# Performance work log

Hardware: AMD Instinct MI355X
Metric: run time of the kernel (lower is better)

The kernel has to match this reference:

```python
import jax, jax.numpy as jnp
import numpy as np

B, T, D, DI, K, M, H, HD, L, VOCAB = 8, 512, 256, 512, 4, 2, 4, 64, 2, 272


def rmsnorm(x, w, eps=1e-6):
    return x * jax.lax.rsqrt(jnp.mean(x * x, axis=-1, keepdims=True) + eps) * w


def rotate_half(x):
    x1, x2 = x[..., ::2], x[..., 1::2]
    return jnp.stack([-x2, x1], axis=-1).reshape(x.shape)


def causal_conv(x, w, b):
    # x: [B,T,C], w: [C,K] depthwise causal conv, then silu
    y = jax.lax.conv_general_dilated(
        x.transpose(0, 2, 1), w[:, None, :],
        window_strides=(1,), padding=[(K - 1, 0)],
        feature_group_count=x.shape[-1])
    return jax.nn.silu(y.transpose(0, 2, 1) + b)


def delta_memory(x, Wv, Wg, Wb, Wa, A_log, dt_bias, Wblend, Wout):
    # x: [B,T,D]; per-timestep delta-rule fast-weight update with decay + key rotation
    Bv, Tn, Dm = x.shape
    vals = (x @ Wv).reshape(Bv, Tn, M, H, HD)
    gate = jax.nn.sigmoid(x @ Wg)                                   # [B,T,H]
    beta = jax.nn.sigmoid(jnp.einsum('btd,mdh->btmh', x, Wb))       # [B,T,M,H]
    alpha = jnp.einsum('btd,mdh->btmh', x, Wa) + dt_bias            # [B,T,M,H]
    decay = jnp.exp(-jnp.exp(A_log)[None, None] * jax.nn.softplus(alpha))
    blend = jax.nn.softmax((x @ Wblend).reshape(Bv, Tn, H, M), axis=-1)
    rk0 = x.reshape(Bv, Tn, H, HD)
    rk0 = rk0 / jnp.maximum(jnp.linalg.norm(rk0, axis=-1, keepdims=True), 1e-12)
    rks = [rk0]
    for _ in range(M - 1):
        rks.append(rotate_half(rks[-1]))
    rks = jnp.stack(rks, axis=2)                                    # [B,T,M,H,d]
    wks = jnp.pad(rks[:, :-1], ((0, 0), (1, 0), (0, 0), (0, 0), (0, 0)))  # shifted keys

    def step(S, inp):
        v, wk, rk, bt, dc, bl, g = inp
        S = S * dc[..., None, None]                                  # [B,M,H,d,d]
        pred = jnp.einsum('bmhdk,bmhd->bmhk', S, wk)
        err = (v - pred) * bt[..., None]
        S = S + wk[..., None] * err[..., None, :]                    # outer-product write
        read = jnp.einsum('bmhdk,bmhd->bmhk', S, rk)
        o = jnp.einsum('bhm,bmhk->bhk', bl, read) * g[..., None]
        return S, o

    tf = lambda a: jnp.moveaxis(a, 1, 0)
    xs = (tf(vals), tf(wks), tf(rks), tf(beta), tf(decay), tf(blend), tf(gate))
    S0 = jnp.zeros((Bv, M, H, HD, HD), x.dtype)
    _, o = jax.lax.scan(step, S0, xs)                                # [T,B,H,d]
    o = jnp.moveaxis(o, 0, 1).reshape(Bv, Tn, Dm)
    return x + o @ Wout


def setup_inputs():
    key = jax.random.key(0)
    ks = jax.random.split(key, 16)
    n = lambda k, shape, sc=0.02: jax.random.normal(k, shape, jnp.float32) * sc
    return {
        'ids': jax.random.randint(ks[0], (B, T), 0, VOCAB, jnp.int32),
        'emb': n(ks[1], (VOCAB, D)),
        'norm_w': jnp.ones((L, D), jnp.float32),
        'W_up': n(ks[2], (L, D, DI)),
        'W_gate': n(ks[3], (L, D, DI)),
        'W_down': n(ks[4], (L, DI, D)),
        'conv_w': n(ks[5], (L, DI, K), 0.1),
        'conv_b': jnp.zeros((L, DI), jnp.float32),
        'Wv': n(ks[6], (L, D, M * D)),
        'Wg': n(ks[7], (L, D, H)),
        'Wb': n(ks[8], (L, M, D, H)),
        'Wa': n(ks[9], (L, M, D, H)),
        'A_log': n(ks[10], (L, M, H), 0.5),
        'dt_bias': n(ks[11], (L, M, H), 0.5),
        'Wblend': n(ks[12], (L, D, H * M)),
        'Wout': n(ks[13], (L, D, D)),
        'final_norm_w': jnp.ones((D,), jnp.float32),
    }


def reference(ids, emb, norm_w, W_up, W_gate, W_down, conv_w, conv_b,
              Wv, Wg, Wb, Wa, A_log, dt_bias, Wblend, Wout, final_norm_w):
    x = emb[ids]
    for l in range(L):
        nx = rmsnorm(x, norm_w[l])
        h = causal_conv(nx @ W_up[l], conv_w[l], conv_b[l])
        out = (jax.nn.silu(nx @ W_gate[l]) * h) @ W_down[l]
        out = delta_memory(out, Wv[l], Wg[l], Wb[l], Wa[l],
                           A_log[l], dt_bias[l], Wblend[l], Wout[l])
        x = x + out
    return rmsnorm(x, final_norm_w) @ emb.T  # tied head
```

## Files before the change

### kernel.cpp

```cpp
#include <hip/hip_runtime.h>
#include <math.h>

#define BB 8
#define TT 512
#define DD 256
#define DIM 512
#define KW 4
#define MM 2
#define HH 4
#define HDIM 64
#define LL 2
#define VV 272

typedef __attribute__((ext_vector_type(8))) short bf16x8;
typedef __attribute__((ext_vector_type(4))) float f32x4;

__device__ __forceinline__ float sigf(float x){ return 1.f/(1.f+__expf(-x)); }
__device__ __forceinline__ float siluf(float x){ return x/(1.f+__expf(-x)); }

__device__ __forceinline__ unsigned short f2bf(float f){
  unsigned int u = __float_as_uint(f);
  unsigned int r = (u + 0x7FFFu + ((u >> 16) & 1u)) >> 16;
  return (unsigned short)r;
}
__device__ __forceinline__ float bf2f(unsigned short s){
  return __uint_as_float(((unsigned int)s) << 16);
}

__device__ __forceinline__ float xor1_add(float x){
  int y = __builtin_amdgcn_update_dpp(0, __float_as_int(x), 0xB1, 0xF, 0xF, true);
  return x + __int_as_float(y);
}
__device__ __forceinline__ float xor2_add(float x){
  int y = __builtin_amdgcn_update_dpp(0, __float_as_int(x), 0x4E, 0xF, 0xF, true);
  return x + __int_as_float(y);
}
__device__ __forceinline__ float ror4_add(float x){
  int y = __builtin_amdgcn_update_dpp(0, __float_as_int(x), 0x124, 0xF, 0xF, true);
  return x + __int_as_float(y);
}
__device__ __forceinline__ float ror8_add(float x){
  int y = __builtin_amdgcn_update_dpp(0, __float_as_int(x), 0x128, 0xF, 0xF, true);
  return x + __int_as_float(y);
}

__device__ __forceinline__ void gl_lds16(const void* g, void* l){
  __builtin_amdgcn_global_load_lds(
      (const __attribute__((address_space(1))) unsigned int*)g,
      (__attribute__((address_space(3))) unsigned int*)l,
      16, 0, 0);
}

#define LWB 589824
__global__ void k_cvt(const float* __restrict__ Wup, const float* __restrict__ Wgate,
                      const float* __restrict__ Wdown, const float* __restrict__ Wv,
                      const float* __restrict__ Wout, const float* __restrict__ emb,
                      const float* __restrict__ normw, const float* __restrict__ fnw,
                      unsigned short* __restrict__ wbf){
  int idx = blockIdx.x*256 + threadIdx.x;
  if (idx >= 2*LWB + VV*DD) return;
  float v;
  if (idx < 2*LWB){
    int l = (idx >= LWB) ? 1 : 0;
    int local = idx - l*LWB;
    if (local < 131072){ int n = local>>8, k = local&255;
      v = Wup[(size_t)l*131072 + k*DIM + n];
      if (l == 1) v *= normw[DD + k]; }
    else if (local < 262144){ local -= 131072; int n = local>>8, k = local&255;
      v = Wgate[(size_t)l*131072 + k*DIM + n];
      if (l == 1) v *= normw[DD + k]; }
    else if (local < 393216){ local -= 262144; int n = local>>9, k = local&511;
      v = Wdown[(size_t)l*131072 + k*DD + n]; }
    else if (local < 524288){ local -= 393216; int n = local>>8, k = local&255;
      v = Wv[(size_t)l*131072 + k*DIM + n]; }
    else { local -= 524288; int n = local>>8, k = local&255;
      v = Wout[(size_t)l*65536 + k*DD + n]; }
  } else {
    int k = (idx - 2*LWB) & 255;
    v = emb[idx - 2*LWB] * fnw[k];
  }
  wbf[idx] = f2bf(v);
}

__global__ void __launch_bounds__(256) k_embed_norm(const int* __restrict__ ids,
                                                    const float* __restrict__ emb,
                                                    const float* __restrict__ w,
                                                    float* __restrict__ x,
                                                    unsigned short* __restrict__ out){
  const int wv = threadIdx.x >> 6, l = threadIdx.x & 63;
  const int row = blockIdx.x*4 + wv;
  float4 v = *(const float4*)&emb[(size_t)ids[row]*DD + l*4];
  *(float4*)&x[(size_t)row*DD + l*4] = v;
  float ss = v.x*v.x + v.y*v.y + v.z*v.z + v.w*v.w;
  #pragma unroll
  for (int o = 32; o > 0; o >>= 1) ss += __shfl_xor(ss, o, 64);
  float sc = rsqrtf(ss*(1.f/DD) + 1e-6f);
  float4 wvv = *(const float4*)&w[l*4];
  ushort4 r;
  r.x = f2bf(v.x*sc*wvv.x); r.y = f2bf(v.y*sc*wvv.y);
  r.z = f2bf(v.z*sc*wvv.z); r.w = f2bf(v.w*sc*wvv.w);
  *(ushort4*)&out[(size_t)row*DD + l*4] = r;
}

template<int MODE>
__global__ void __launch_bounds__(256) k_gemm64(const unsigned short* __restrict__ A,
                                                const unsigned short* __restrict__ Bt,
                                                float* __restrict__ Cf,
                                                unsigned short* __restrict__ Cb,
                                                int N, int K){
  __shared__ unsigned short as[64][72];
  __shared__ unsigned short bs[64][72];
  const int tid = threadIdx.x;
  const int w = tid >> 6, l = tid & 63;
  const int m0 = blockIdx.y*64, n0 = blockIdx.x*64;
  const int ar = tid >> 2, ac = (tid & 3)*16;
  f32x4 acc[4] = {};
  for (int k0 = 0; k0 < K; k0 += 64){
    { const bf16x8* src = (const bf16x8*)&A[(size_t)(m0+ar)*K + k0 + ac];
      *(bf16x8*)&as[ar][ac]   = src[0];
      *(bf16x8*)&as[ar][ac+8] = src[1];
    }
    { int n = n0 + ar;
      bf16x8 z; z = (bf16x8)(short)0;
      bf16x8 b0 = z, b1 = z;
      if (n < N){
        const bf16x8* src = (const bf16x8*)&Bt[(size_t)n*K + k0 + ac];
        b0 = src[0]; b1 = src[1];
      }
      *(bf16x8*)&bs[ar][ac]   = b0;
      *(bf16x8*)&bs[ar][ac+8] = b1;
    }
    __syncthreads();
    const int mr = w*16 + (l & 15);
    const int kb = (l >> 4)*8;
    #pragma unroll
    for (int kc2 = 0; kc2 < 2; ++kc2){
      bf16x8 af = *(const bf16x8*)&as[mr][kc2*32 + kb];
      #pragma unroll
      for (int nt = 0; nt < 4; ++nt){
        bf16x8 bfr = *(const bf16x8*)&bs[nt*16 + (l & 15)][kc2*32 + kb];
        acc[nt] = __builtin_amdgcn_mfma_f32_16x16x32_bf16(af, bfr, acc[nt], 0, 0, 0);
      }
    }
    __syncthreads();
  }
  #pragma unroll
  for (int nt = 0; nt < 4; ++nt){
    int col = n0 + nt*16 + (l & 15);
    if (col < N){
      #pragma unroll
      for (int r = 0; r < 4; ++r){
        int row = m0 + w*16 + (l >> 4)*4 + r;
        if (MODE == 0 || MODE == 2) Cf[(size_t)row*N + col] = acc[nt][r];
        if (MODE == 1 || MODE == 2) Cb[(size_t)row*N + col] = f2bf(acc[nt][r]);
      }
    }
  }
}

__global__ void __launch_bounds__(256) k_gemmlogit(const float* __restrict__ X,
                                                   const float* __restrict__ pssq,
                                                   const unsigned short* __restrict__ Bt,
                                                   float* __restrict__ Cf,
                                                   int N, int K){
  __shared__ unsigned short as[64][72];
  __shared__ unsigned short bs[64][72];
  const int tid = threadIdx.x;
  const int w = tid >> 6, l = tid & 63;
  const int m0 = blockIdx.y*64, n0 = blockIdx.x*64;
  const int ar = tid >> 2, ac = (tid & 3)*16;
  const int arow = m0 + ar;
  const int ROWS = BB*TT;
  float ssq = pssq[arow] + pssq[ROWS + arow] + pssq[2*ROWS + arow] + pssq[3*ROWS + arow];
  const float sc = rsqrtf(ssq*(1.f/DD) + 1e-6f);
  f32x4 acc[4] = {};
  for (int k0 = 0; k0 < K; k0 += 64){
    { const float* src = &X[(size_t)arow*K + k0 + ac];
      #pragma unroll
      for (int j = 0; j < 4; ++j){
        float4 a = *(const float4*)&src[j*4];
        ushort4 u = make_ushort4(f2bf(a.x*sc), f2bf(a.y*sc), f2bf(a.z*sc), f2bf(a.w*sc));
        *(ushort4*)&as[ar][ac + j*4] = u;
      }
    }
    { int n = n0 + ar;
      bf16x8 z; z = (bf16x8)(short)0;
      bf16x8 b0 = z, b1 = z;
      if (n < N){
        const bf16x8* src = (const bf16x8*)&Bt[(size_t)n*K + k0 + ac];
        b0 = src[0]; b1 = src[1];
      }
      *(bf16x8*)&bs[ar][ac]   = b0;
      *(bf16x8*)&bs[ar][ac+8] = b1;
    }
    __syncthreads();
    const int mr = w*16 + (l & 15);
    const int kb = (l >> 4)*8;
    #pragma unroll
    for (int kc2 = 0; kc2 < 2; ++kc2){
      bf16x8 af = *(const bf16x8*)&as[mr][kc2*32 + kb];
      #pragma unroll
      for (int nt = 0; nt < 4; ++nt){
        bf16x8 bfr = *(const bf16x8*)&bs[nt*16 + (l & 15)][kc2*32 + kb];
        acc[nt] = __builtin_amdgcn_mfma_f32_16x16x32_bf16(af, bfr, acc[nt], 0, 0, 0);
      }
    }
    __syncthreads();
  }
  #pragma unroll
  for (int nt = 0; nt < 4; ++nt){
    int col = n0 + nt*16 + (l & 15);
    if (col < N){
      #pragma unroll
      for (int r = 0; r < 4; ++r){
        int row = m0 + w*16 + (l >> 4)*4 + r;
        Cf[(size_t)row*N + col] = acc[nt][r];
      }
    }
  }
}

template<int MODE>
__global__ void __launch_bounds__(256) k_gemm128(const unsigned short* __restrict__ A,
                                                 const unsigned short* __restrict__ Bt,
                                                 float* __restrict__ Cf,
                                                 unsigned short* __restrict__ Cb,
                                                 int N, int K){
  __shared__ unsigned short as[128][72];
  __shared__ unsigned short bs[64][72];
  const int tid = threadIdx.x;
  const int w = tid >> 6, l = tid & 63;
  const int m0 = blockIdx.y*128, n0 = blockIdx.x*64;
  const int ar = tid >> 1, ac = (tid & 1)*32;
  const int br = tid >> 2, bc = (tid & 3)*16;
  f32x4 acc[2][4] = {};
  for (int k0 = 0; k0 < K; k0 += 64){
    { const bf16x8* src = (const bf16x8*)&A[(size_t)(m0+ar)*K + k0 + ac];
      *(bf16x8*)&as[ar][ac]    = src[0];
      *(bf16x8*)&as[ar][ac+8]  = src[1];
      *(bf16x8*)&as[ar][ac+16] = src[2];
      *(bf16x8*)&as[ar][ac+24] = src[3];
    }
    { int n = n0 + br;
      bf16x8 z; z = (bf16x8)(short)0;
      bf16x8 b0 = z, b1 = z;
      if (n < N){
        const bf16x8* s = (const bf16x8*)&Bt[(size_t)n*K + k0 + bc];
        b0 = s[0]; b1 = s[1];
      }
      *(bf16x8*)&bs[br][bc]   = b0;
      *(bf16x8*)&bs[br][bc+8] = b1;
    }
    __syncthreads();
    const int lr = l & 15, kb = (l >> 4)*8;
    #pragma unroll
    for (int kc2 = 0; kc2 < 2; ++kc2){
      bf16x8 af0 = *(const bf16x8*)&as[w*32 + lr][kc2*32 + kb];
      bf16x8 af1 = *(const bf16x8*)&as[w*32 + 16 + lr][kc2*32 + kb];
      #pragma unroll
      for (int nt = 0; nt < 4; ++nt){
        bf16x8 bfr = *(const bf16x8*)&bs[nt*16 + lr][kc2*32 + kb];
        acc[0][nt] = __builtin_amdgcn_mfma_f32_16x16x32_bf16(af0, bfr, acc[0][nt], 0, 0, 0);
        acc[1][nt] = __builtin_amdgcn_mfma_f32_16x16x32_bf16(af1, bfr, acc[1][nt], 0, 0, 0);
      }
    }
    __syncthreads();
  }
  const int lr = l & 15;
  #pragma unroll
  for (int mt = 0; mt < 2; ++mt){
    #pragma unroll
    for (int nt = 0; nt < 4; ++nt){
      int col = n0 + nt*16 + lr;
      if (col < N){
        #pragma unroll
        for (int r = 0; r < 4; ++r){
          int row = m0 + w*32 + mt*16 + (l >> 4)*4 + r;
          if (MODE == 0 || MODE == 2) Cf[(size_t)row*N + col] = acc[mt][nt][r];
          if (MODE == 1 || MODE == 2) Cb[(size_t)row*N + col] = f2bf(acc[mt][nt][r]);
        }
      }
    }
  }
}

template<int L>
__global__ void __launch_bounds__(256) k_gemm_upc(
    const unsigned short* __restrict__ Anyb,
    const float* __restrict__ X, const float* __restrict__ pssq,
    const unsigned short* __restrict__ But,
    const unsigned short* __restrict__ Bgt,
    const float* __restrict__ cw, const float* __restrict__ cb,
    unsigned short* __restrict__ Chh)
{
  __shared__ unsigned short as[128][72];
  __shared__ unsigned short bu[64][72];
  __shared__ unsigned short bg[64][72];
  __shared__ unsigned short s_ub[132][68];
  __shared__ float s_cw[64][4];
  __shared__ float s_cb[64];
  const int tid = threadIdx.x;
  const int w = tid >> 6, l = tid & 63;
  const int m0 = blockIdx.y*128, n0 = blockIdx.x*64;
  const int ar = tid >> 1, ac = (tid & 1)*32;
  const int br = tid >> 2, bc = (tid & 3)*16;
  const int ROWS = BB*TT;
  const int t0 = m0 & (TT-1);

  float scA = 1.f;
  if (L == 1){
    const int arow = m0 + ar;
    float ssq = pssq[arow] + pssq[ROWS + arow] + pssq[2*ROWS + arow] + pssq[3*ROWS + arow];
    scA = rsqrtf(ssq*(1.f/DD) + 1e-6f);
  }

  if (tid < 192){
    int i = tid >> 6;
    int c = tid & 63;
    float acc = 0.f;
    if (t0 != 0){
      int grow = m0 - 3 + i;
      const unsigned short* bptr = &But[(size_t)(n0+c)*DD];
      if (L == 0){
        const unsigned short* a = &Anyb[(size_t)grow*DD];
        for (int k = 0; k < DD; k += 8){
          bf16x8 av = *(const bf16x8*)&a[k];
          bf16x8 bv = *(const bf16x8*)&bptr[k];
          #pragma unroll
          for (int e = 0; e < 8; ++e)
            acc = fmaf(bf2f((unsigned short)av[e]), bf2f((unsigned short)bv[e]), acc);
        }
      } else {
        float ssq = pssq[grow] + pssq[ROWS + grow] + pssq[2*ROWS + grow] + pssq[3*ROWS + grow];
        float sc = rsqrtf(ssq*(1.f/DD) + 1e-6f);
        const float* a = &X[(size_t)grow*DD];
        for (int k = 0; k < DD; k += 4){
          float4 av = *(const float4*)&a[k];
          #pragma unroll
          for (int e = 0; e < 4; ++e){
            float ae = bf2f(f2bf(((const float*)&av)[e]*sc));
            acc = fmaf(ae, bf2f(bptr[k+e]), acc);
          }
        }
      }
    }
    s_ub[tid >> 6][tid & 63] = (t0 != 0) ? f2bf(acc) : (unsigned short)0;
  }
  if (tid < 64){
    *(float4*)&s_cw[tid][0] = *(const float4*)&cw[(n0+tid)*KW];
    s_cb[tid] = cb[n0+tid];
  }

  f32x4 accu[2][4] = {}; f32x4 accg[2][4] = {};
  for (int k0 = 0; k0 < DD; k0 += 64){
    if (L == 0){
      const bf16x8* src = (const bf16x8*)&Anyb[(size_t)(m0+ar)*DD + k0 + ac];
      *(bf16x8*)&as[ar][ac]    = src[0];
      *(bf16x8*)&as[ar][ac+8]  = src[1];
      *(bf16x8*)&as[ar][ac+16] = src[2];
      *(bf16x8*)&as[ar][ac+24] = src[3];
    } else {
      const float* src = &X[(size_t)(m0+ar)*DD + k0 + ac];
      #pragma unroll
      for (int j = 0; j < 8; ++j){
        float4 a = *(const float4*)&src[j*4];
        ushort4 u = make_ushort4(f2bf(a.x*scA), f2bf(a.y*scA), f2bf(a.z*scA), f2bf(a.w*scA));
        *(ushort4*)&as[ar][ac + j*4] = u;
      }
    }
    { const bf16x8* s0 = (const bf16x8*)&But[(size_t)(n0+br)*DD + k0 + bc];
      *(bf16x8*)&bu[br][bc]   = s0[0];
      *(bf16x8*)&bu[br][bc+8] = s0[1];
      const bf16x8* s1 = (const bf16x8*)&Bgt[(size_t)(n0+br)*DD + k0 + bc];
      *(bf16x8*)&bg[br][bc]   = s1[0];
      *(bf16x8*)&bg[br][bc+8] = s1[1];
    }
    __syncthreads();
    const int lr = l & 15, kb = (l >> 4)*8;
    #pragma unroll
    for (int kc2 = 0; kc2 < 2; ++kc2){
      bf16x8 af0 = *(const bf16x8*)&as[w*32 + lr][kc2*32 + kb];
      bf16x8 af1 = *(const bf16x8*)&as[w*32 + 16 + lr][kc2*32 + kb];
      #pragma unroll
      for (int nt = 0; nt < 4; ++nt){
        bf16x8 b0 = *(const bf16x8*)&bu[nt*16 + lr][kc2*32 + kb];
        accu[0][nt] = __builtin_amdgcn_mfma_f32_16x16x32_bf16(af0, b0, accu[0][nt], 0, 0, 0);
        accu[1][nt] = __builtin_amdgcn_mfma_f32_16x16x32_bf16(af1, b0, accu[1][nt], 0, 0, 0);
        bf16x8 b1 = *(const bf16x8*)&bg[nt*16 + lr][kc2*32 + kb];
        accg[0][nt] = __builtin_amdgcn_mfma_f32_16x16x32_bf16(af0, b1, accg[0][nt], 0, 0, 0);
        accg[1][nt] = __builtin_amdgcn_mfma_f32_16x16x32_bf16(af1, b1, accg[1][nt], 0, 0, 0);
      }
    }
    __syncthreads();
  }

  const int lr = l & 15;
  #pragma unroll
  for (int mt = 0; mt < 2; ++mt)
    #pragma unroll
    for (int nt = 0; nt < 4; ++nt)
      #pragma unroll
      for (int r = 0; r < 4; ++r){
        int trow = w*32 + mt*16 + (l >> 4)*4 + r;
        s_ub[3 + trow][nt*16 + lr] = f2bf(accu[mt][nt][r]);
      }
  __syncthreads();

  #pragma unroll
  for (int mt = 0; mt < 2; ++mt)
    #pragma unroll
    for (int nt = 0; nt < 4; ++nt)
      #pragma unroll
      for (int r = 0; r < 4; ++r){
        int trow = w*32 + mt*16 + (l >> 4)*4 + r;
        int cl = nt*16 + lr;
        float a0 = s_cb[cl];
        #pragma unroll
        for (int j = 0; j < KW; ++j)
          a0 = fmaf(bf2f(s_ub[trow + j][cl]), s_cw[cl][j], a0);
        float h = siluf(a0);
        float o = siluf(accg[mt][nt][r]) * h;
        Chh[(size_t)(m0 + trow)*DIM + (n0 + cl)] = f2bf(o);
      }
}

__global__ void __launch_bounds__(256) k_gemm_wout(const float* __restrict__ p0,
                                                   const float* __restrict__ p1,
                                                   const unsigned short* __restrict__ Bt,
                                                   const float* __restrict__ y,
                                                   float* __restrict__ x,
                                                   float* __restrict__ rowssq){
  __shared__ unsigned short as[64][72];
  __shared__ unsigned short bs[64][72];
  const int tid = threadIdx.x;
  const int w = tid >> 6, l = tid & 63;
  const int m0 = blockIdx.y*64, n0 = blockIdx.x*64;
  const int ar = tid >> 2, ac = (tid & 3)*16;
  f32x4 acc[4] = {};
  for (int k0 = 0; k0 < DD; k0 += 64){
    #pragma unroll
    for (int j = 0; j < 4; ++j){
      size_t off = (size_t)(m0+ar)*DD + k0 + ac + j*4;
      float4 a = *(const float4*)&p0[off];
      float4 b = *(const float4*)&p1[off];
      a.x += b.x; a.y += b.y; a.z += b.z; a.w += b.w;
      ushort4 u = make_ushort4(f2bf(a.x), f2bf(a.y), f2bf(a.z), f2bf(a.w));
      *(ushort4*)&as[ar][ac + j*4] = u;
    }
    { const bf16x8* src = (const bf16x8*)&Bt[(size_t)(n0+ar)*DD + k0 + ac];
      *(bf16x8*)&bs[ar][ac]   = src[0];
      *(bf16x8*)&bs[ar][ac+8] = src[1];
    }
    __syncthreads();
    const int mr = w*16 + (l & 15);
    const int kb = (l >> 4)*8;
    #pragma unroll
    for (int kc2 = 0; kc2 < 2; ++kc2){
      bf16x8 af = *(const bf16x8*)&as[mr][kc2*32 + kb];
      #pragma unroll
      for (int nt = 0; nt < 4; ++nt){
        bf16x8 bfr = *(const bf16x8*)&bs[nt*16 + (l & 15)][kc2*32 + kb];
        acc[nt] = __builtin_amdgcn_mfma_f32_16x16x32_bf16(af, bfr, acc[nt], 0, 0, 0);
      }
    }
    __syncthreads();
  }
  const int ROWS = BB*TT;
  float ssq[4] = {0.f, 0.f, 0.f, 0.f};
  #pragma unroll
  for (int nt = 0; nt < 4; ++nt){
    int col = n0 + nt*16 + (l & 15);
    #pragma unroll
    for (int r = 0; r < 4; ++r){
      int row = m0 + w*16 + (l >> 4)*4 + r;
      size_t off = (size_t)row*DD + col;
      float nv = x[off] + y[off] + acc[nt][r];
      x[off] = nv;
      ssq[r] = fmaf(nv, nv, ssq[r]);
    }
  }
  #pragma unroll
  for (int r = 0; r < 4; ++r){
    float s = ssq[r];
    s = xor1_add(s); s = xor2_add(s); s = ror4_add(s); s = ror8_add(s);
    if ((l & 15) == 0){
      int row = m0 + w*16 + (l >> 4)*4 + r;
      rowssq[(size_t)blockIdx.x*ROWS + row] = s;
    }
  }
}

__global__ void __launch_bounds__(256) k_fused(const float* __restrict__ y,
    const float* __restrict__ Wg, const float* __restrict__ Wb,
    const float* __restrict__ Wa, const float* __restrict__ Wbl,
    const float* __restrict__ A_log, const float* __restrict__ dtb,
    float* __restrict__ rkb, float* __restrict__ scal){
  __shared__ float s_y[4][260];
  __shared__ float s_p[4][32];
  const int wv = threadIdx.x >> 6, l = threadIdx.x & 63;
  const int row = blockIdx.x*4 + wv;

  float4 yv = *(const float4*)&y[(size_t)row*DD + l*4];
  *(float4*)&s_y[wv][l*4] = yv;

  float ss = yv.x*yv.x + yv.y*yv.y + yv.z*yv.z + yv.w*yv.w;
  ss = xor1_add(ss); ss = xor2_add(ss);
  ss = ror4_add(ss); ss = ror8_add(ss);
  float inv = 1.f / fmaxf(sqrtf(ss), 1e-12f);
  float4 rv; rv.x = yv.x*inv; rv.y = yv.y*inv; rv.z = yv.z*inv; rv.w = yv.w*inv;
  *(float4*)&rkb[(size_t)row*DD + l*4] = rv;

  __syncthreads();

  const int j = (l < 28) ? l : 27;
  const float* wp; int stride;
  if (j < 4){ wp = Wg + j; stride = HH; }
  else if (j < 12){ int m=(j-4)>>2, h=(j-4)&3; wp = Wb + (size_t)m*DD*HH + h; stride = HH; }
  else if (j < 20){ int m=(j-12)>>2, h=(j-12)&3; wp = Wa + (size_t)m*DD*HH + h; stride = HH; }
  else { wp = Wbl + (j-20); stride = HH*MM; }
  float a0=0.f,a1=0.f,a2=0.f,a3=0.f;
  #pragma unroll 4
  for (int k = 0; k < DD; k += 4){
    a0 = fmaf(s_y[wv][k+0], wp[(k+0)*stride], a0);
    a1 = fmaf(s_y[wv][k+1], wp[(k+1)*stride], a1);
    a2 = fmaf(s_y[wv][k+2], wp[(k+2)*stride], a2);
    a3 = fmaf(s_y[wv][k+3], wp[(k+3)*stride], a3);
  }
  if (l < 28) s_p[wv][l] = (a0+a1)+(a2+a3);

  __syncthreads();

  if (l < 8){
    int m = l >> 2, h = l & 3;
    float gs  = sigf(s_p[wv][h]);
    float btv = sigf(s_p[wv][4 + m*4 + h]);
    float sp  = s_p[wv][12 + m*4 + h] + dtb[m*HH + h];
    sp = (sp > 15.f) ? sp : log1pf(__expf(sp));
    float dc  = __expf(-__expf(A_log[m*HH + h]) * sp);
    float l0 = s_p[wv][20 + h*2], l1 = s_p[wv][20 + h*2 + 1];
    float mx = fmaxf(l0, l1);
    float e0 = __expf(l0-mx), e1 = __expf(l1-mx);
    float bl = (m ? e1 : e0) / (e0 + e1);
    float4 o; o.x = dc; o.y = btv; o.z = bl*gs; o.w = 0.f;
    *(float4*)&scal[((size_t)row*MM + m)*(HH*4) + h*4] = o;
  }
}

#define SSTEP(T_, WK, RK, PF, VB, SB) { \
  const float dc = SB.x, btv = SB.y, blg = SB.z; \
  const float v = VB; \
  { const int tn_ = ((T_)+2 < 64) ? (T_)+2 : 63; \
    PF = *(const float4*)&s_rk[p][tn_][dbase]; \
    VB = bf2f(s_v[p][tn_][vidx]); \
    SB = *(const float4*)&s_sc[p][tn_][0]; } \
  const float err = (v - dc*rrc)*btv; \
  float rr0=0.f, rr1=0.f; \
  { const float4 rp = WK; const float4 rc = RK; \
    float w0,w1,w2,w3,c0,c1,c2,c3; \
    if (ROT == 0){ w0=rp.x; w1=rp.y; w2=rp.z; w3=rp.w; c0=rc.x; c1=rc.y; c2=rc.z; c3=rc.w; } \
    else { w0=-rp.y; w1=rp.x; w2=-rp.w; w3=rp.z; c0=-rc.y; c1=rc.x; c2=-rc.w; c3=rc.z; } \
    S[0] = fmaf(S[0], dc, w0*err); rr0 = fmaf(S[0], c0, rr0); \
    S[1] = fmaf(S[1], dc, w1*err); rr1 = fmaf(S[1], c1, rr1); \
    S[2] = fmaf(S[2], dc, w2*err); rr0 = fmaf(S[2], c2, rr0); \
    S[3] = fmaf(S[3], dc, w3*err); rr1 = fmaf(S[3], c3, rr1); } \
  float rr = rr0 + rr1; \
  rr = xor1_add(rr); rr = xor2_add(rr); rr = ror4_add(rr); rr = ror8_add(rr); \
  rrc = rr; \
  if (seg == 0) part[(size_t)(rowchunk + (T_))*DD + h*HDIM + kq4*4 + klocal] = blg*rr; \
}

template<int ROT>
__device__ __forceinline__ void scan_body(int b, int h, int kq4, int l,
    const unsigned short* __restrict__ vals, const float* __restrict__ rkb,
    const float* __restrict__ scal, float* __restrict__ part,
    float (*s_rk)[64][64], unsigned short (*s_v)[64][8], float (*s_sc)[64][4])
{
  const int seg = l & 15, klocal = l >> 4;
  const int dbase = seg*4;
  const int vidx = (kq4 & 1)*4 + klocal;
  const int kq8 = kq4 >> 1;
  const int rowbase = b*TT;

  float S[4];
  #pragma unroll
  for (int j = 0; j < 4; ++j) S[j] = 0.f;
  const float4 Z = make_float4(0.f,0.f,0.f,0.f);
  float4 rb0 = Z, rb1 = Z, rb2 = Z, rb3 = Z;
  float vb0 = 0.f, vb1 = 0.f;
  float4 sb0 = Z, sb1 = Z;
  float rrc = 0.f;

  auto stage = [&](int c, int pbuf){
    const int r0 = rowbase + c*64;
    #pragma unroll
    for (int i = 0; i < 16; ++i){
      const float* g = rkb + (size_t)(r0 + i*4 + (l>>4))*DD + h*HDIM + (l&15)*4;
      gl_lds16(g, &s_rk[pbuf][i*4][0]);
    }
    { const unsigned short* g = vals + ((size_t)(r0 + l)*MM + ROT)*DD + h*HDIM + kq8*8;
      gl_lds16(g, &s_v[pbuf][0][0]); }
    { const float* g = scal + ((size_t)(r0 + l)*MM + ROT)*(HH*4) + h*4;
      gl_lds16(g, &s_sc[pbuf][0][0]); }
  };

  stage(0, 0);
  for (int c = 0; c < TT/64; ++c){
    const int p = c & 1;
    __syncthreads();
    if (c + 1 < TT/64) stage(c+1, p^1);
    rb0 = *(const float4*)&s_rk[p][0][dbase];
    rb1 = *(const float4*)&s_rk[p][1][dbase];
    vb0 = bf2f(s_v[p][0][vidx]); vb1 = bf2f(s_v[p][1][vidx]);
    sb0 = *(const float4*)&s_sc[p][0][0]; sb1 = *(const float4*)&s_sc[p][1][0];
    const int rowchunk = rowbase + c*64;
    for (int tt = 0; tt < 64; tt += 4){
      SSTEP(tt+0, rb3, rb0, rb2, vb0, sb0)
      SSTEP(tt+1, rb0, rb1, rb3, vb1, sb1)
      SSTEP(tt+2, rb1, rb2, rb0, vb0, sb0)
      SSTEP(tt+3, rb2, rb3, rb1, vb1, sb1)
    }
  }
}

__global__ void __launch_bounds__(64) k_scan(const unsigned short* __restrict__ vals,
                                             const float* __restrict__ rkb,
                                             const float* __restrict__ scal,
                                             float* __restrict__ partials){
  __shared__ float s_rk[2][64][64];
  __shared__ unsigned short s_v[2][64][8];
  __shared__ float s_sc[2][64][4];
  const int bi = blockIdx.x;
  const int kq4 = bi & 15;
  const int m  = (bi >> 4) & 1;
  const int h  = (bi >> 5) & 3;
  const int b  = bi >> 7;
  float* part = partials + (size_t)m*(BB*TT*DD);
  if (m == 0) scan_body<0>(b, h, kq4, threadIdx.x, vals, rkb, scal, part, s_rk, s_v, s_sc);
  else        scan_body<1>(b, h, kq4, threadIdx.x, vals, rkb, scal, part, s_rk, s_v, s_sc);
}

extern "C" void kernel_launch(void* const* d_in, const int* in_sizes, int n_in,
                              void* d_out, int out_size, void* d_ws, size_t ws_size,
                              hipStream_t stream){
  const int*   ids   = (const int*)d_in[0];
  const float* emb   = (const float*)d_in[1];
  const float* normw = (const float*)d_in[2];
  const float* Wup   = (const float*)d_in[3];
  const float* Wgate = (const float*)d_in[4];
  const float* Wdown = (const float*)d_in[5];
  const float* convw = (const float*)d_in[6];
  const float* convb = (const float*)d_in[7];
  const float* Wv    = (const float*)d_in[8];
  const float* Wg    = (const float*)d_in[9];
  const float* Wb    = (const float*)d_in[10];
  const float* Wa    = (const float*)d_in[11];
  const float* A_log = (const float*)d_in[12];
  const float* dtb   = (const float*)d_in[13];
  const float* Wbl   = (const float*)d_in[14];
  const float* Wout  = (const float*)d_in[15];
  const float* fnw   = (const float*)d_in[16];
  float* out = (float*)d_out;

  const int ROWS = BB*TT;
  const size_t MEG = 1u << 20;
  float* ws   = (float*)d_ws;
  float* x    = ws;
  unsigned short* nyb = (unsigned short*)(x + MEG);
  float* big1 = x + MEG + MEG/2;
  float* big2 = big1 + 2*MEG;
  float* y    = big2 + 2*MEG;
  float* rkb  = y    + MEG;
  float* scal = rkb  + MEG;
  float* rowssq = scal + (1u<<17);
  unsigned short* wbf = (unsigned short*)(rowssq + 4*ROWS);

  unsigned short* gb  = (unsigned short*)(big1 + MEG);
  unsigned short* valsb = (unsigned short*)big1;

  { int total = 2*LWB + VV*DD;
    k_cvt<<<(total + 255)/256, 256, 0, stream>>>(Wup, Wgate, Wdown, Wv, Wout, emb,
                                                 normw, fnw, wbf); }

  k_embed_norm<<<ROWS/4, 256, 0, stream>>>(ids, emb, normw, x, nyb);

  for (int l = 0; l < LL; ++l){
    unsigned short* wl = wbf + (size_t)l*LWB;
    unsigned short* upT   = wl;
    unsigned short* gateT = wl + 131072;
    unsigned short* downT = wl + 262144;
    unsigned short* wvT   = wl + 393216;
    unsigned short* woutT = wl + 524288;

    if (l == 0)
      k_gemm_upc<0><<<dim3(DIM/64, ROWS/128), 256, 0, stream>>>(
          nyb, nullptr, nullptr, upT, gateT, convw + l*DIM*KW, convb + l*DIM, gb);
    else
      k_gemm_upc<1><<<dim3(DIM/64, ROWS/128), 256, 0, stream>>>(
          nullptr, x, rowssq, upT, gateT, convw + l*DIM*KW, convb + l*DIM, gb);
    k_gemm64<2><<<dim3(DD/64, ROWS/64), 256, 0, stream>>>(gb, downT, y, nyb, DD, DIM);
    k_gemm128<1><<<dim3(DIM/64, ROWS/128), 256, 0, stream>>>(nyb, wvT, nullptr, valsb, DIM, DD);
    k_fused<<<ROWS/4, 256, 0, stream>>>(y, Wg + l*DD*HH, Wb + (size_t)l*MM*DD*HH,
                                        Wa + (size_t)l*MM*DD*HH, Wbl + l*DD*HH*MM,
                                        A_log + l*MM*HH, dtb + l*MM*HH, rkb, scal);
    k_scan<<<BB*HH*MM*16, 64, 0, stream>>>(valsb, rkb, scal, big2);
    k_gemm_wout<<<dim3(DD/64, ROWS/64), 256, 0, stream>>>(big2, big2 + MEG, woutT, y, x, rowssq);
  }

  unsigned short* embT = wbf + 2*LWB;
  k_gemmlogit<<<dim3((VV+63)/64, ROWS/64), 256, 0, stream>>>(x, rowssq, embT, out, VV, DD);
}
```

Baseline: 274.5 us.

## Merge independent kernels into combined launches and precompute scan step coefficients

The weight conversion and embedding-norm kernels now run as one launch, with blocks partitioned by index. The Wv value GEMM and the per-row scalar projection kernel run as one launch in the same way, so one launch and its tail are removed per layer. The scan step now premultiplies v*beta and decay*beta when prefetching, which shortens the dependent arithmetic chain inside the recurrence. Merged kernels share one LDS size and register budget, which may lower occupancy for the lighter half.

Result: faster. 263.3 us (median of 2 runs) (-4.1%).

```diff
diff --git a/kernel.cpp b/kernel.cpp
--- a/kernel.cpp
+++ b/kernel.cpp
@@ -52,54 +52,54 @@
 }
 
 #define LWB 589824
-__global__ void k_cvt(const float* __restrict__ Wup, const float* __restrict__ Wgate,
-                      const float* __restrict__ Wdown, const float* __restrict__ Wv,
-                      const float* __restrict__ Wout, const float* __restrict__ emb,
-                      const float* __restrict__ normw, const float* __restrict__ fnw,
-                      unsigned short* __restrict__ wbf){
-  int idx = blockIdx.x*256 + threadIdx.x;
-  if (idx >= 2*LWB + VV*DD) return;
-  float v;
-  if (idx < 2*LWB){
-    int l = (idx >= LWB) ? 1 : 0;
-    int local = idx - l*LWB;
-    if (local < 131072){ int n = local>>8, k = local&255;
-      v = Wup[(size_t)l*131072 + k*DIM + n];
-      if (l == 1) v *= normw[DD + k]; }
-    else if (local < 262144){ local -= 131072; int n = local>>8, k = local&255;
-      v = Wgate[(size_t)l*131072 + k*DIM + n];
-      if (l == 1) v *= normw[DD + k]; }
-    else if (local < 393216){ local -= 262144; int n = local>>9, k = local&511;
-      v = Wdown[(size_t)l*131072 + k*DD + n]; }
-    else if (local < 524288){ local -= 393216; int n = local>>8, k = local&255;
-      v = Wv[(size_t)l*131072 + k*DIM + n]; }
-    else { local -= 524288; int n = local>>8, k = local&255;
-      v = Wout[(size_t)l*65536 + k*DD + n]; }
+#define CVTB 4880
+__global__ void __launch_bounds__(256) k_init(
+    const float* __restrict__ Wup, const float* __restrict__ Wgate,
+    const float* __restrict__ Wdown, const float* __restrict__ Wv,
+    const float* __restrict__ Wout, const float* __restrict__ emb,
+    const float* __restrict__ normw, const float* __restrict__ fnw,
+    unsigned short* __restrict__ wbf,
+    const int* __restrict__ ids, float* __restrict__ x,
+    unsigned short* __restrict__ nyb){
+  if (blockIdx.x < CVTB){
+    int idx = blockIdx.x*256 + threadIdx.x;
+    if (idx >= 2*LWB + VV*DD) return;
+    float v;
+    if (idx < 2*LWB){
+      int l = (idx >= LWB) ? 1 : 0;
+      int local = idx - l*LWB;
+      if (local < 131072){ int n = local>>8, k = local&255;
+        v = Wup[(size_t)l*131072 + k*DIM + n];
+        if (l == 1) v *= normw[DD + k]; }
+      else if (local < 262144){ local -= 131072; int n = local>>8, k = local&255;
+        v = Wgate[(size_t)l*131072 + k*DIM + n];
+        if (l == 1) v *= normw[DD + k]; }
+      else if (local < 393216){ local -= 262144; int n = local>>9, k = local&511;
+        v = Wdown[(size_t)l*131072 + k*DD + n]; }
+      else if (local < 524288){ local -= 393216; int n = local>>8, k = local&255;
+        v = Wv[(size_t)l*131072 + k*DIM + n]; }
+      else { local -= 524288; int n = local>>8, k = local&255;
+        v = Wout[(size_t)l*65536 + k*DD + n]; }
+    } else {
+      int k = (idx - 2*LWB) & 255;
+      v = emb[idx - 2*LWB] * fnw[k];
+    }
+    wbf[idx] = f2bf(v);
   } else {
-    int k = (idx - 2*LWB) & 255;
-    v = emb[idx - 2*LWB] * fnw[k];
-  }
-  wbf[idx] = f2bf(v);
-}
-
-__global__ void __launch_bounds__(256) k_embed_norm(const int* __restrict__ ids,
-                                                    const float* __restrict__ emb,
-                                                    const float* __restrict__ w,
-                                                    float* __restrict__ x,
-                                                    unsigned short* __restrict__ out){
-  const int wv = threadIdx.x >> 6, l = threadIdx.x & 63;
-  const int row = blockIdx.x*4 + wv;
-  float4 v = *(const float4*)&emb[(size_t)ids[row]*DD + l*4];
-  *(float4*)&x[(size_t)row*DD + l*4] = v;
-  float ss = v.x*v.x + v.y*v.y + v.z*v.z + v.w*v.w;
-  #pragma unroll
-  for (int o = 32; o > 0; o >>= 1) ss += __shfl_xor(ss, o, 64);
-  float sc = rsqrtf(ss*(1.f/DD) + 1e-6f);
-  float4 wvv = *(const float4*)&w[l*4];
-  ushort4 r;
-  r.x = f2bf(v.x*sc*wvv.x); r.y = f2bf(v.y*sc*wvv.y);
-  r.z = f2bf(v.z*sc*wvv.z); r.w = f2bf(v.w*sc*wvv.w);
-  *(ushort4*)&out[(size_t)row*DD + l*4] = r;
+    const int wv = threadIdx.x >> 6, l = threadIdx.x & 63;
+    const int row = (blockIdx.x - CVTB)*4 + wv;
+    float4 v = *(const float4*)&emb[(size_t)ids[row]*DD + l*4];
+    *(float4*)&x[(size_t)row*DD + l*4] = v;
+    float ss = v.x*v.x + v.y*v.y + v.z*v.z + v.w*v.w;
+    #pragma unroll
+    for (int o = 32; o > 0; o >>= 1) ss += __shfl_xor(ss, o, 64);
+    float sc = rsqrtf(ss*(1.f/DD) + 1e-6f);
+    float4 wvv = *(const float4*)&normw[l*4];
+    ushort4 r;
+    r.x = f2bf(v.x*sc*wvv.x); r.y = f2bf(v.y*sc*wvv.y);
+    r.z = f2bf(v.z*sc*wvv.z); r.w = f2bf(v.w*sc*wvv.w);
+    *(ushort4*)&nyb[(size_t)row*DD + l*4] = r;
+  }
 }
 
 template<int MODE>
@@ -220,66 +220,112 @@
   }
 }
 
-template<int MODE>
-__global__ void __launch_bounds__(256) k_gemm128(const unsigned short* __restrict__ A,
-                                                 const unsigned short* __restrict__ Bt,
-                                                 float* __restrict__ Cf,
-                                                 unsigned short* __restrict__ Cb,
-                                                 int N, int K){
-  __shared__ unsigned short as[128][72];
-  __shared__ unsigned short bs[64][72];
+__global__ void __launch_bounds__(256) k_wvf(
+    const unsigned short* __restrict__ A, const unsigned short* __restrict__ Bt,
+    unsigned short* __restrict__ Cb,
+    const float* __restrict__ y,
+    const float* __restrict__ Wg, const float* __restrict__ Wb,
+    const float* __restrict__ Wa, const float* __restrict__ Wbl,
+    const float* __restrict__ A_log, const float* __restrict__ dtb,
+    float* __restrict__ rkb, float* __restrict__ scal)
+{
+  __shared__ __align__(16) unsigned char smem[27648];
   const int tid = threadIdx.x;
-  const int w = tid >> 6, l = tid & 63;
-  const int m0 = blockIdx.y*128, n0 = blockIdx.x*64;
-  const int ar = tid >> 1, ac = (tid & 1)*32;
-  const int br = tid >> 2, bc = (tid & 3)*16;
-  f32x4 acc[2][4] = {};
-  for (int k0 = 0; k0 < K; k0 += 64){
-    { const bf16x8* src = (const bf16x8*)&A[(size_t)(m0+ar)*K + k0 + ac];
-      *(bf16x8*)&as[ar][ac]    = src[0];
-      *(bf16x8*)&as[ar][ac+8]  = src[1];
-      *(bf16x8*)&as[ar][ac+16] = src[2];
-      *(bf16x8*)&as[ar][ac+24] = src[3];
-    }
-    { int n = n0 + br;
-      bf16x8 z; z = (bf16x8)(short)0;
-      bf16x8 b0 = z, b1 = z;
-      if (n < N){
-        const bf16x8* s = (const bf16x8*)&Bt[(size_t)n*K + k0 + bc];
-        b0 = s[0]; b1 = s[1];
-      }
-      *(bf16x8*)&bs[br][bc]   = b0;
-      *(bf16x8*)&bs[br][bc+8] = b1;
-    }
-    __syncthreads();
-    const int lr = l & 15, kb = (l >> 4)*8;
-    #pragma unroll
-    for (int kc2 = 0; kc2 < 2; ++kc2){
-      bf16x8 af0 = *(const bf16x8*)&as[w*32 + lr][kc2*32 + kb];
-      bf16x8 af1 = *(const bf16x8*)&as[w*32 + 16 + lr][kc2*32 + kb];
+  if (blockIdx.x < 256){
+    unsigned short (*as)[72] = (unsigned short (*)[72])smem;
+    unsigned short (*bs)[72] = (unsigned short (*)[72])(smem + 128*72*2);
+    const int w = tid >> 6, l = tid & 63;
+    const int m0 = (blockIdx.x >> 3)*128, n0 = (blockIdx.x & 7)*64;
+    const int ar = tid >> 1, ac = (tid & 1)*32;
+    const int br = tid >> 2, bc = (tid & 3)*16;
+    f32x4 acc[2][4] = {};
+    for (int k0 = 0; k0 < DD; k0 += 64){
+      { const bf16x8* src = (const bf16x8*)&A[(size_t)(m0+ar)*DD + k0 + ac];
+        *(bf16x8*)&as[ar][ac]    = src[0];
+        *(bf16x8*)&as[ar][ac+8]  = src[1];
+        *(bf16x8*)&as[ar][ac+16] = src[2];
+        *(bf16x8*)&as[ar][ac+24] = src[3];
+      }
+      { const bf16x8* s = (const bf16x8*)&Bt[(size_t)(n0+br)*DD + k0 + bc];
+        *(bf16x8*)&bs[br][bc]   = s[0];
+        *(bf16x8*)&bs[br][bc+8] = s[1];
+      }
+      __syncthreads();
+      const int lr = l & 15, kb = (l >> 4)*8;
+      #pragma unroll
+      for (int kc2 = 0; kc2 < 2; ++kc2){
+        bf16x8 af0 = *(const bf16x8*)&as[w*32 + lr][kc2*32 + kb];
+        bf16x8 af1 = *(const bf16x8*)&as[w*32 + 16 + lr][kc2*32 + kb];
+        #pragma unroll
+        for (int nt = 0; nt < 4; ++nt){
+          bf16x8 bfr = *(const bf16x8*)&bs[nt*16 + lr][kc2*32 + kb];
+          acc[0][nt] = __builtin_amdgcn_mfma_f32_16x16x32_bf16(af0, bfr, acc[0][nt], 0, 0, 0);
+          acc[1][nt] = __builtin_amdgcn_mfma_f32_16x16x32_bf16(af1, bfr, acc[1][nt], 0, 0, 0);
+        }
+      }
+      __syncthreads();
+    }
+    const int lr = l & 15;
+    #pragma unroll
+    for (int mt = 0; mt < 2; ++mt)
       #pragma unroll
       for (int nt = 0; nt < 4; ++nt){
-        bf16x8 bfr = *(const bf16x8*)&bs[nt*16 + lr][kc2*32 + kb];
-        acc[0][nt] = __builtin_amdgcn_mfma_f32_16x16x32_bf16(af0, bfr, acc[0][nt], 0, 0, 0);
-        acc[1][nt] = __builtin_amdgcn_mfma_f32_16x16x32_bf16(af1, bfr, acc[1][nt], 0, 0, 0);
-      }
-    }
-    __syncthreads();
-  }
-  const int lr = l & 15;
-  #pragma unroll
-  for (int mt = 0; mt < 2; ++mt){
-    #pragma unroll
-    for (int nt = 0; nt < 4; ++nt){
-      int col = n0 + nt*16 + lr;
-      if (col < N){
+        int col = n0 + nt*16 + lr;
         #pragma unroll
         for (int r = 0; r < 4; ++r){
           int row = m0 + w*32 + mt*16 + (l >> 4)*4 + r;
-          if (MODE == 0 || MODE == 2) Cf[(size_t)row*N + col] = acc[mt][nt][r];
-          if (MODE == 1 || MODE == 2) Cb[(size_t)row*N + col] = f2bf(acc[mt][nt][r]);
+          Cb[(size_t)row*DIM + col] = f2bf(acc[mt][nt][r]);
         }
       }
+  } else {
+    float (*s_y)[260] = (float (*)[260])smem;
+    float (*s_p)[32]  = (float (*)[32])(smem + 4*260*4);
+    const int wv = tid >> 6, l = tid & 63;
+    const int row = (blockIdx.x - 256)*4 + wv;
+
+    float4 yv = *(const float4*)&y[(size_t)row*DD + l*4];
+    *(float4*)&s_y[wv][l*4] = yv;
+
+    float ss = yv.x*yv.x + yv.y*yv.y + yv.z*yv.z + yv.w*yv.w;
+    ss = xor1_add(ss); ss = xor2_add(ss);
+    ss = ror4_add(ss); ss = ror8_add(ss);
+    float inv = 1.f / fmaxf(sqrtf(ss), 1e-12f);
+    float4 rv; rv.x = yv.x*inv; rv.y = yv.y*inv; rv.z = yv.z*inv; rv.w = yv.w*inv;
+    *(float4*)&rkb[(size_t)row*DD + l*4] = rv;
+
+    __syncthreads();
+
+    const int j = (l < 28) ? l : 27;
+    const float* wp; int stride;
+    if (j < 4){ wp = Wg + j; stride = HH; }
+    else if (j < 12){ int m=(j-4)>>2, h=(j-4)&3; wp = Wb + (size_t)m*DD*HH + h; stride = HH; }
+    else if (j < 20){ int m=(j-12)>>2, h=(j-12)&3; wp = Wa + (size_t)m*DD*HH + h; stride = HH; }
+    else { wp = Wbl + (j-20); stride = HH*MM; }
+    float a0=0.f,a1=0.f,a2=0.f,a3=0.f;
+    #pragma unroll 4
+    for (int k = 0; k < DD; k += 4){
+      a0 = fmaf(s_y[wv][k+0], wp[(k+0)*stride], a0);
+      a1 = fmaf(s_y[wv][k+1], wp[(k+1)*stride], a1);
+      a2 = fmaf(s_y[wv][k+2], wp[(k+2)*stride], a2);
+      a3 = fmaf(s_y[wv][k+3], wp[(k+3)*stride], a3);
+    }
+    if (l < 28) s_p[wv][l] = (a0+a1)+(a2+a3);
+
+    __syncthreads();
+
+    if (l < 8){
+      int m = l >> 2, h = l & 3;
+      float gs  = sigf(s_p[wv][h]);
+      float btv = sigf(s_p[wv][4 + m*4 + h]);
+      float sp  = s_p[wv][12 + m*4 + h] + dtb[m*HH + h];
+      sp = (sp > 15.f) ? sp : log1pf(__expf(sp));
+      float dc  = __expf(-__expf(A_log[m*HH + h]) * sp);
+      float l0 = s_p[wv][20 + h*2], l1 = s_p[wv][20 + h*2 + 1];
+      float mx = fmaxf(l0, l1);
+      float e0 = __expf(l0-mx), e1 = __expf(l1-mx);
+      float bl = (m ? e1 : e0) / (e0 + e1);
+      float4 o; o.x = dc; o.y = btv; o.z = bl*gs; o.w = 0.f;
+      *(float4*)&scal[((size_t)row*MM + m)*(HH*4) + h*4] = o;
     }
   }
 }
@@ -490,83 +536,27 @@
   }
 }
 
-__global__ void __launch_bounds__(256) k_fused(const float* __restrict__ y,
-    const float* __restrict__ Wg, const float* __restrict__ Wb,
-    const float* __restrict__ Wa, const float* __restrict__ Wbl,
-    const float* __restrict__ A_log, const float* __restrict__ dtb,
-    float* __restrict__ rkb, float* __restrict__ scal){
-  __shared__ float s_y[4][260];
-  __shared__ float s_p[4][32];
-  const int wv = threadIdx.x >> 6, l = threadIdx.x & 63;
-  const int row = blockIdx.x*4 + wv;
-
-  float4 yv = *(const float4*)&y[(size_t)row*DD + l*4];
-  *(float4*)&s_y[wv][l*4] = yv;
-
-  float ss = yv.x*yv.x + yv.y*yv.y + yv.z*yv.z + yv.w*yv.w;
-  ss = xor1_add(ss); ss = xor2_add(ss);
-  ss = ror4_add(ss); ss = ror8_add(ss);
-  float inv = 1.f / fmaxf(sqrtf(ss), 1e-12f);
-  float4 rv; rv.x = yv.x*inv; rv.y = yv.y*inv; rv.z = yv.z*inv; rv.w = yv.w*inv;
-  *(float4*)&rkb[(size_t)row*DD + l*4] = rv;
-
-  __syncthreads();
-
-  const int j = (l < 28) ? l : 27;
-  const float* wp; int stride;
-  if (j < 4){ wp = Wg + j; stride = HH; }
-  else if (j < 12){ int m=(j-4)>>2, h=(j-4)&3; wp = Wb + (size_t)m*DD*HH + h; stride = HH; }
-  else if (j < 20){ int m=(j-12)>>2, h=(j-12)&3; wp = Wa + (size_t)m*DD*HH + h; stride = HH; }
-  else { wp = Wbl + (j-20); stride = HH*MM; }
-  float a0=0.f,a1=0.f,a2=0.f,a3=0.f;
-  #pragma unroll 4
-  for (int k = 0; k < DD; k += 4){
-    a0 = fmaf(s_y[wv][k+0], wp[(k+0)*stride], a0);
-    a1 = fmaf(s_y[wv][k+1], wp[(k+1)*stride], a1);
-    a2 = fmaf(s_y[wv][k+2], wp[(k+2)*stride], a2);
-    a3 = fmaf(s_y[wv][k+3], wp[(k+3)*stride], a3);
-  }
-  if (l < 28) s_p[wv][l] = (a0+a1)+(a2+a3);
-
-  __syncthreads();
-
-  if (l < 8){
-    int m = l >> 2, h = l & 3;
-    float gs  = sigf(s_p[wv][h]);
-    float btv = sigf(s_p[wv][4 + m*4 + h]);
-    float sp  = s_p[wv][12 + m*4 + h] + dtb[m*HH + h];
-    sp = (sp > 15.f) ? sp : log1pf(__expf(sp));
-    float dc  = __expf(-__expf(A_log[m*HH + h]) * sp);
-    float l0 = s_p[wv][20 + h*2], l1 = s_p[wv][20 + h*2 + 1];
-    float mx = fmaxf(l0, l1);
-    float e0 = __expf(l0-mx), e1 = __expf(l1-mx);
-    float bl = (m ? e1 : e0) / (e0 + e1);
-    float4 o; o.x = dc; o.y = btv; o.z = bl*gs; o.w = 0.f;
-    *(float4*)&scal[((size_t)row*MM + m)*(HH*4) + h*4] = o;
-  }
-}
-
-#define SSTEP(T_, WK, RK, PF, VB, SB) { \
-  const float dc = SB.x, btv = SB.y, blg = SB.z; \
-  const float v = VB; \
+#define SSTEP(T_, WK, RK, PF, VB, DB, DC, BL) { \
+  const float vbt = VB, dcb = DB, dcl = DC, blgl = BL; \
   { const int tn_ = ((T_)+2 < 64) ? (T_)+2 : 63; \
     PF = *(const float4*)&s_rk[p][tn_][dbase]; \
-    VB = bf2f(s_v[p][tn_][vidx]); \
-    SB = *(const float4*)&s_sc[p][tn_][0]; } \
-  const float err = (v - dc*rrc)*btv; \
+    float vraw = bf2f(s_v[p][tn_][vidx]); \
+    float4 sc4 = *(const float4*)&s_sc[p][tn_][0]; \
+    VB = vraw*sc4.y; DB = sc4.x*sc4.y; DC = sc4.x; BL = sc4.z; } \
+  const float err = fmaf(-dcb, rrc, vbt); \
   float rr0=0.f, rr1=0.f; \
   { const float4 rp = WK; const float4 rc = RK; \
     float w0,w1,w2,w3,c0,c1,c2,c3; \
     if (ROT == 0){ w0=rp.x; w1=rp.y; w2=rp.z; w3=rp.w; c0=rc.x; c1=rc.y; c2=rc.z; c3=rc.w; } \
     else { w0=-rp.y; w1=rp.x; w2=-rp.w; w3=rp.z; c0=-rc.y; c1=rc.x; c2=-rc.w; c3=rc.z; } \
-    S[0] = fmaf(S[0], dc, w0*err); rr0 = fmaf(S[0], c0, rr0); \
-    S[1] = fmaf(S[1], dc, w1*err); rr1 = fmaf(S[1], c1, rr1); \
-    S[2] = fmaf(S[2], dc, w2*err); rr0 = fmaf(S[2], c2, rr0); \
-    S[3] = fmaf(S[3], dc, w3*err); rr1 = fmaf(S[3], c3, rr1); } \
+    S[0] = fmaf(S[0], dcl, w0*err); rr0 = fmaf(S[0], c0, rr0); \
+    S[1] = fmaf(S[1], dcl, w1*err); rr1 = fmaf(S[1], c1, rr1); \
+    S[2] = fmaf(S[2], dcl, w2*err); rr0 = fmaf(S[2], c2, rr0); \
+    S[3] = fmaf(S[3], dcl, w3*err); rr1 = fmaf(S[3], c3, rr1); } \
   float rr = rr0 + rr1; \
   rr = xor1_add(rr); rr = xor2_add(rr); rr = ror4_add(rr); rr = ror8_add(rr); \
   rrc = rr; \
-  if (seg == 0) part[(size_t)(rowchunk + (T_))*DD + h*HDIM + kq4*4 + klocal] = blg*rr; \
+  if (seg == 0) part[(size_t)(rowchunk + (T_))*DD + h*HDIM + kq4*4 + klocal] = blgl*rr; \
 }
 
 template<int ROT>
@@ -586,8 +576,7 @@
   for (int j = 0; j < 4; ++j) S[j] = 0.f;
   const float4 Z = make_float4(0.f,0.f,0.f,0.f);
   float4 rb0 = Z, rb1 = Z, rb2 = Z, rb3 = Z;
-  float vb0 = 0.f, vb1 = 0.f;
-  float4 sb0 = Z, sb1 = Z;
+  float vb0=0.f, vb1=0.f, db0=0.f, db1=0.f, dc0=0.f, dc1=0.f, bl0=0.f, bl1=0.f;
   float rrc = 0.f;
 
   auto stage = [&](int c, int pbuf){
@@ -610,14 +599,18 @@
     if (c + 1 < TT/64) stage(c+1, p^1);
     rb0 = *(const float4*)&s_rk[p][0][dbase];
     rb1 = *(const float4*)&s_rk[p][1][dbase];
-    vb0 = bf2f(s_v[p][0][vidx]); vb1 = bf2f(s_v[p][1][vidx]);
-    sb0 = *(const float4*)&s_sc[p][0][0]; sb1 = *(const float4*)&s_sc[p][1][0];
+    { float vraw = bf2f(s_v[p][0][vidx]);
+      float4 sc4 = *(const float4*)&s_sc[p][0][0];
+      vb0 = vraw*sc4.y; db0 = sc4.x*sc4.y; dc0 = sc4.x; bl0 = sc4.z; }
+    { float vraw = bf2f(s_v[p][1][vidx]);
+      float4 sc4 = *(const float4*)&s_sc[p][1][0];
+      vb1 = vraw*sc4.y; db1 = sc4.x*sc4.y; dc1 = sc4.x; bl1 = sc4.z; }
     const int rowchunk = rowbase + c*64;
     for (int tt = 0; tt < 64; tt += 4){
-      SSTEP(tt+0, rb3, rb0, rb2, vb0, sb0)
-      SSTEP(tt+1, rb0, rb1, rb3, vb1, sb1)
-      SSTEP(tt+2, rb1, rb2, rb0, vb0, sb0)
-      SSTEP(tt+3, rb2, rb3, rb1, vb1, sb1)
+      SSTEP(tt+0, rb3, rb0, rb2, vb0, db0, dc0, bl0)
+      SSTEP(tt+1, rb0, rb1, rb3, vb1, db1, dc1, bl1)
+      SSTEP(tt+2, rb1, rb2, rb0, vb0, db0, dc0, bl0)
+      SSTEP(tt+3, rb2, rb3, rb1, vb1, db1, dc1, bl1)
     }
   }
 }
@@ -677,11 +670,8 @@
   unsigned short* gb  = (unsigned short*)(big1 + MEG);
   unsigned short* valsb = (unsigned short*)big1;
 
-  { int total = 2*LWB + VV*DD;
-    k_cvt<<<(total + 255)/256, 256, 0, stream>>>(Wup, Wgate, Wdown, Wv, Wout, emb,
-                                                 normw, fnw, wbf); }
-
-  k_embed_norm<<<ROWS/4, 256, 0, stream>>>(ids, emb, normw, x, nyb);
+  k_init<<<CVTB + ROWS/4, 256, 0, stream>>>(Wup, Wgate, Wdown, Wv, Wout, emb,
+                                            normw, fnw, wbf, ids, x, nyb);
 
   for (int l = 0; l < LL; ++l){
     unsigned short* wl = wbf + (size_t)l*LWB;
@@ -698,10 +688,10 @@
       k_gemm_upc<1><<<dim3(DIM/64, ROWS/128), 256, 0, stream>>>(
           nullptr, x, rowssq, upT, gateT, convw + l*DIM*KW, convb + l*DIM, gb);
     k_gemm64<2><<<dim3(DD/64, ROWS/64), 256, 0, stream>>>(gb, downT, y, nyb, DD, DIM);
-    k_gemm128<1><<<dim3(DIM/64, ROWS/128), 256, 0, stream>>>(nyb, wvT, nullptr, valsb, DIM, DD);
-    k_fused<<<ROWS/4, 256, 0, stream>>>(y, Wg + l*DD*HH, Wb + (size_t)l*MM*DD*HH,
-                                        Wa + (size_t)l*MM*DD*HH, Wbl + l*DD*HH*MM,
-                                        A_log + l*MM*HH, dtb + l*MM*HH, rkb, scal);
+    k_wvf<<<256 + ROWS/4, 256, 0, stream>>>(nyb, wvT, valsb, y,
+                                            Wg + l*DD*HH, Wb + (size_t)l*MM*DD*HH,
+                                            Wa + (size_t)l*MM*DD*HH, Wbl + l*DD*HH*MM,
+                                            A_log + l*MM*HH, dtb + l*MM*HH, rkb, scal);
     k_scan<<<BB*HH*MM*16, 64, 0, stream>>>(valsb, rkb, scal, big2);
     k_gemm_wout<<<dim3(DD/64, ROWS/64), 256, 0, stream>>>(big2, big2 + MEG, woutT, y, x, rowssq);
   }
```
